# Kernel optimization log

Hardware: AMD Instinct MI355X
Metric: run time of the kernel (lower is better)

## Reference

```python
import jax, jax.numpy as jnp
import numpy as np

SIZE = 1024      # codebook entries
CODE_DIM = 256   # embedding dim


def setup_inputs() -> dict:
    key = jax.random.key(0)
    k_z, k_w = jax.random.split(key)
    z = jax.random.normal(k_z, (8, CODE_DIM, 16, 32, 32), dtype=jnp.float32)
    # init.uniform_(weight, -1/size, 1/size)
    codebook = jax.random.uniform(
        k_w, (SIZE, CODE_DIM), dtype=jnp.float32,
        minval=-1.0 / SIZE, maxval=1.0 / SIZE)
    return {"z": z, "codebook": codebook}


def reference(z, codebook):
    bs, d, t, h, w = z.shape
    # tokens: [N, d] with N = bs*t*h*w (matches permute(0,2,3,4,1).reshape(-1,d))
    zf = jnp.transpose(z, (0, 2, 3, 4, 1)).reshape(-1, d)
    # squared-distance expansion instead of materializing [size, N, d]:
    # ||z - e||^2 = ||z||^2 - 2 z.e + ||e||^2 ; argmin identical to argmin of norm
    d2 = (jnp.sum(zf * zf, axis=1, keepdims=True)
          - 2.0 * (zf @ codebook.T)
          + jnp.sum(codebook * codebook, axis=1))  # [N, size]
    encoding_indices = jnp.argmin(d2, axis=-1).reshape(bs, t, h, w)
    # gather + permute back to [bs, d, t, h, w]
    quantized = jnp.transpose(codebook[encoding_indices], (0, 4, 1, 2, 3))
    st = z + jax.lax.stop_gradient(quantized - z)  # straight-through output
    return (quantized, st, encoding_indices)
```

## Files before the change

### kernel.cpp

```cpp
#include <hip/hip_runtime.h>
#include <stdint.h>


constexpr int Dd  = 256;
constexpr int SPB = 16384;
constexpr int Nn  = 131072;
constexpr int Kk  = 1024;
constexpr int CCAP = 16;
#define WWIN 2.2e-3f

typedef short short8 __attribute__((ext_vector_type(8)));
typedef float v4f    __attribute__((ext_vector_type(4)));

__device__ __forceinline__ unsigned bf16pk(float a, float b){
  unsigned ua = __float_as_uint(a), ub = __float_as_uint(b);
  ua = (ua + 0x7fffu + ((ua >> 16) & 1u)) >> 16;
  ub = (ub + 0x7fffu + ((ub >> 16) & 1u)) & 0xffff0000u;
  return ua | ub;
}
__device__ __forceinline__ short8 frg(uint4 u){
  union { uint4 a; short8 b; } x; x.a = u; return x.b;
}
__device__ __forceinline__ v4f mfma16(short8 a, short8 b, v4f c){
  return __builtin_amdgcn_mfma_f32_16x16x32_bf16(a, b, c, 0, 0, 0);
}
__device__ __forceinline__ void dma16(const void* g, void* l){
  __builtin_amdgcn_global_load_lds((const __attribute__((address_space(1))) void*)g,
                                   (__attribute__((address_space(3))) void*)l, 16, 0, 0);
}

__global__ __launch_bounds__(64) void cnorm_k(const float* __restrict__ cb,
                                              float* __restrict__ cn){
  const int k = blockIdx.x, l = threadIdx.x;
  const float* row = cb + (size_t)k * Dd;
  float s = 0.f;
  #pragma unroll
  for (int c = 0; c < Dd; c += 64){ float v = row[c + l]; s += v * v; }
  #pragma unroll
  for (int off = 32; off > 0; off >>= 1) s += __shfl_down(s, off, 64);
  if (l == 0) cn[k] = s;
}

__global__ __launch_bounds__(256) void cconv_k(const float* __restrict__ cb,
                                               uint4* __restrict__ Bg){
  const int cc = blockIdx.x, n = threadIdx.x;
  const float* row = cb + (size_t)(cc * 256 + n) * Dd;
  for (int dc = 0; dc < 8; dc++){
    float v[32];
    const float4* rp = (const float4*)(row + dc * 32);
    #pragma unroll
    for (int q = 0; q < 8; q++){
      float4 f = rp[q]; v[4*q]=f.x; v[4*q+1]=f.y; v[4*q+2]=f.z; v[4*q+3]=f.w;
    }
    unsigned hv[16];
    #pragma unroll
    for (int p = 0; p < 16; p++) hv[p] = bf16pk(v[2*p], v[2*p+1]);
    size_t base = ((size_t)cc * 8 + dc) * 1024;
    #pragma unroll
    for (int kq = 0; kq < 4; kq++)
      Bg[base + (size_t)kq*256 + n] = make_uint4(hv[4*kq],hv[4*kq+1],hv[4*kq+2],hv[4*kq+3]);
  }
}

__device__ __forceinline__ void epi(const v4f (&acc)[4], const int c,
                                    const int li, const int lq, const int w,
                                    const int tok0, const float* cnS,
                                    unsigned (&bestR)[4], unsigned (&thrU)[4],
                                    int (&cntR)[4],
                                    unsigned short* __restrict__ candW){
  float cnv[4];
  #pragma unroll
  for (int ni = 0; ni < 4; ni++) cnv[ni] = cnS[c*64 + ni*16 + li];
  const int codeB = c*64 + li;
  #pragma unroll
  for (int r = 0; r < 4; r++){
    unsigned pv[4];
    unsigned pm = 0xFFFFFFFFu;
    #pragma unroll
    for (int ni = 0; ni < 4; ni++){
      float s = fmaf(acc[ni][r], -2.0f, cnv[ni]);
      unsigned u = __float_as_uint(s);
      u ^= (unsigned)((int)u >> 31) | 0x80000000u;
      unsigned p = (u & 0xFFFFFC00u) | (unsigned)(codeB + ni*16);
      pv[ni] = p;
      pm = (pm < p) ? pm : p;
    }
    unsigned pmw = pm;
    #pragma unroll
    for (int off = 1; off < 16; off <<= 1){
      unsigned o = (unsigned)__shfl_xor((int)pmw, off, 16);
      pmw = (pmw < o) ? pmw : o;
    }
    if (pmw <= bestR[r]){
      bestR[r] = pmw;
      unsigned bp = pmw & 0xFFFFFC00u;
      unsigned fb = (bp & 0x80000000u) ? (bp ^ 0x80000000u) : ~bp;
      float thrf = __uint_as_float(fb) + WWIN;
      unsigned tu = __float_as_uint(thrf);
      tu ^= (unsigned)((int)tu >> 31) | 0x80000000u;
      thrU[r] = tu | 1023u;
    }
    if (__any(pm <= thrU[r])){
      const int tok = tok0 + w*16 + lq*4 + r;
      int base = cntR[r];
      #pragma unroll
      for (int ni = 0; ni < 4; ni++){
        const unsigned p = pv[ni];
        const bool pass = (p <= thrU[r]);
        unsigned long long bal = __ballot(pass);
        const unsigned bq = (unsigned)(bal >> (lq*16)) & 0xFFFFu;
        if (pass){
          int pos = base + __popc(bq & ((1u << li) - 1u));
          if (pos < CCAP)
            candW[(size_t)tok*CCAP + pos] = (unsigned short)(p & 1023u);
        }
        base += __popc(bq);
      }
      cntR[r] = base;
    }
  }
}

__global__ __launch_bounds__(512, 4) void vq_sweep_k(const float* __restrict__ z,
                                                     const uint4* __restrict__ Bg,
                                                     const float* __restrict__ cnG,
                                                     int* __restrict__ cntW,
                                                     unsigned short* __restrict__ candW,
                                                     int* __restrict__ abestW,
                                                     int* __restrict__ hCntB,
                                                     int* __restrict__ heavyRegion,
                                                     int* __restrict__ idsW,
                                                     float* __restrict__ out){
  __shared__ uint4 Bs[2][2048];
  __shared__ float cnS[1024];
  __shared__ int hN;
  __shared__ int hT[128];

  const int tid = threadIdx.x, bId = blockIdx.x;
  const int w = tid >> 6, ln = tid & 63;
  const int li = ln & 15, lq = ln >> 4;

  if (tid == 0) hN = 0;

  if (w < 4) dma16((const uint4*)cnG + w*64 + ln, (uint4*)&cnS[w*256]);
  int bOff[4];
  #pragma unroll
  for (int j = 0; j < 4; j++){
    const int f = j*512 + tid;
    bOff[j] = (f >> 8)*1024 + ((f >> 6) & 3)*256 + (f & 63);
  }
  #pragma unroll
  for (int j = 0; j < 4; j++)
    dma16(Bg + bOff[j], &Bs[0][j*512 + w*64]);

  const int tok0 = bId * 128;
  const int b = tok0 >> 14;
  const int s0 = tok0 & 16383;
  const float* zb = z + (size_t)b * Dd * SPB + s0;
  short8 aF[8];
  const int tl = w*16 + li;
  #pragma unroll
  for (int kk = 0; kk < 8; kk++){
    float v[8];
    #pragma unroll
    for (int j = 0; j < 8; j++)
      v[j] = zb[(size_t)(kk*32 + lq*8 + j) * SPB + tl];
    union { unsigned u[4]; short8 s8; } x;
    #pragma unroll
    for (int p = 0; p < 4; p++) x.u[p] = bf16pk(v[2*p], v[2*p+1]);
    aF[kk] = x.s8;
  }

  unsigned bestR[4], thrU[4]; int cntR[4];
  #pragma unroll
  for (int i = 0; i < 4; i++){ bestR[i] = 0xFFFFFFFFu; thrU[i] = 0u; cntR[i] = 0; }

  v4f accA[4], accB[4];
  const v4f vz = {0.f, 0.f, 0.f, 0.f};

  for (int cp = 0; cp < 8; cp++){
    const int c0 = cp*2, c1 = c0 + 1;

    {
      const int cn1 = c0 + 1;
      const int srcB = (cn1 >> 2)*8192 + (cn1 & 3)*64;
      #pragma unroll
      for (int j = 0; j < 4; j++)
        dma16(Bg + srcB + bOff[j], &Bs[1][j*512 + w*64]);
      asm volatile("s_waitcnt vmcnt(4)" ::: "memory");
      __builtin_amdgcn_s_barrier();
      asm volatile("" ::: "memory");

      #pragma unroll
      for (int ni = 0; ni < 4; ni++) accA[ni] = vz;
      const uint4* Bbase = &Bs[0][lq*64 + li];
      __builtin_amdgcn_s_setprio(1);
      #pragma unroll
      for (int kk = 0; kk < 8; kk++){
        short8 b0 = frg(Bbase[kk*256 +  0]);
        short8 b1 = frg(Bbase[kk*256 + 16]);
        short8 b2 = frg(Bbase[kk*256 + 32]);
        short8 b3 = frg(Bbase[kk*256 + 48]);
        accA[0] = mfma16(aF[kk], b0, accA[0]);
        accA[1] = mfma16(aF[kk], b1, accA[1]);
        accA[2] = mfma16(aF[kk], b2, accA[2]);
        accA[3] = mfma16(aF[kk], b3, accA[3]);
      }
      __builtin_amdgcn_s_setprio(0);
      if (cp)
        epi(accB, c0 - 1, li, lq, w, tok0, cnS, bestR, thrU, cntR, candW);
      __builtin_amdgcn_s_barrier();
      asm volatile("" ::: "memory");
    }

    {
      if (c1 < 15){
        const int cn1 = c1 + 1;
        const int srcB = (cn1 >> 2)*8192 + (cn1 & 3)*64;
        #pragma unroll
        for (int j = 0; j < 4; j++)
          dma16(Bg + srcB + bOff[j], &Bs[0][j*512 + w*64]);
        asm volatile("s_waitcnt vmcnt(4)" ::: "memory");
      } else {
        asm volatile("s_waitcnt vmcnt(0)" ::: "memory");
      }
      __builtin_amdgcn_s_barrier();
      asm volatile("" ::: "memory");

      #pragma unroll
      for (int ni = 0; ni < 4; ni++) accB[ni] = vz;
      const uint4* Bbase = &Bs[1][lq*64 + li];
      __builtin_amdgcn_s_setprio(1);
      #pragma unroll
      for (int kk = 0; kk < 8; kk++){
        short8 b0 = frg(Bbase[kk*256 +  0]);
        short8 b1 = frg(Bbase[kk*256 + 16]);
        short8 b2 = frg(Bbase[kk*256 + 32]);
        short8 b3 = frg(Bbase[kk*256 + 48]);
        accB[0] = mfma16(aF[kk], b0, accB[0]);
        accB[1] = mfma16(aF[kk], b1, accB[1]);
        accB[2] = mfma16(aF[kk], b2, accB[2]);
        accB[3] = mfma16(aF[kk], b3, accB[3]);
      }
      __builtin_amdgcn_s_setprio(0);
      epi(accA, c0, li, lq, w, tok0, cnS, bestR, thrU, cntR, candW);
      __builtin_amdgcn_s_barrier();
      asm volatile("" ::: "memory");
    }
  }
  epi(accB, 15, li, lq, w, tok0, cnS, bestR, thrU, cntR, candW);

  if (li == 0){
    #pragma unroll
    for (int r = 0; r < 4; r++){
      const int tok = tok0 + w*16 + lq*4 + r;
      if (cntR[r] == 1){
        const int code = (int)(bestR[r] & 1023u);
        idsW[tok] = code;
        out[(size_t)2 * Nn * Dd + tok] = (float)code;
      } else {
        int p = atomicAdd(&hN, 1);
        hT[p] = tok;
        cntW[tok] = cntR[r];
        abestW[tok] = (int)(bestR[r] & 1023u);
      }
    }
  }
  __syncthreads();
  if (tid == 0) hCntB[bId] = hN;
  if (tid < hN) heavyRegion[bId*128 + tid] = hT[tid];
}

__global__ __launch_bounds__(256) void vq_finish_k(const float* __restrict__ z,
                                                   const float* __restrict__ cb,
                                                   const float* __restrict__ cnG,
                                                   const int* __restrict__ cntW,
                                                   const unsigned short* __restrict__ candW,
                                                   const int* __restrict__ abestW,
                                                   const int* __restrict__ hCntB,
                                                   const int* __restrict__ heavyRegion,
                                                   const int* __restrict__ idsW,
                                                   float* __restrict__ out){
  __shared__ __align__(16) float smem[64*129];
  __shared__ int idS[128];

  const int tid = threadIdx.x, reg = blockIdx.x;
  const int tok0 = reg * 128;
  const int b = tok0 >> 14, sb = tok0 & 16383;

  if (tid < 128) idS[tid] = idsW[tok0 + tid];

  const int h = hCntB[reg];
  if (h > 0){
    float* zS = smem;
    const float* zb = z + (size_t)b * Dd * SPB + sb;

    const bool act = tid < h;
    int tok = 0, tl = 0, n = 0, abest = 0;
    bool ovf = false;
    unsigned short cds[CCAP];
    if (act){
      tok = heavyRegion[reg*128 + tid];
      tl = tok & 127;
      n = cntW[tok];
      ovf = (n > CCAP);
      if (ovf) n = CCAP;
      *(uint4*)&cds[0] = *(const uint4*)&candW[(size_t)tok * CCAP];
      *(uint4*)&cds[8] = *(const uint4*)&candW[(size_t)tok * CCAP + 8];
      abest = abestW[tok];
    }
    const int eIdx = act ? (ovf ? abest : (int)cds[0]) : 0;

    float accs[CCAP];
    #pragma unroll
    for (int i = 0; i < CCAP; i++) accs[i] = 0.f;
    float accE = 0.f, za = 0.f;

    for (int ch = 0; ch < 4; ch++){
      if (ch) __syncthreads();
      #pragma unroll
      for (int rr = 0; rr < 8; rr++){
        const int f4 = rr*256 + tid;
        const int row = f4 >> 5, c4 = f4 & 31;
        const float4 v = *(const float4*)(zb + (size_t)(ch*64 + row) * SPB + c4*4);
        *(float4*)&zS[row*128 + c4*4] = v;
      }
      __syncthreads();
      if (act){
        #pragma unroll 8
        for (int d = 0; d < 64; d++){
          const float v = zS[d*128 + tl];
          za = fmaf(v, v, za);
        }
        #pragma unroll
        for (int ci = 0; ci < CCAP; ci++){
          if (ci < n){
            const float* cr = cb + (size_t)cds[ci] * Dd + ch*64;
            float a = accs[ci];
            #pragma unroll
            for (int d = 0; d < 64; d += 4){
              const float4 cv = *(const float4*)(cr + d);
              a = fmaf(zS[(d+0)*128 + tl], cv.x, a);
              a = fmaf(zS[(d+1)*128 + tl], cv.y, a);
              a = fmaf(zS[(d+2)*128 + tl], cv.z, a);
              a = fmaf(zS[(d+3)*128 + tl], cv.w, a);
            }
            accs[ci] = a;
          }
        }
        if (ovf){
          const float* cr = cb + (size_t)eIdx * Dd + ch*64;
          float a = accE;
          #pragma unroll
          for (int d = 0; d < 64; d += 4){
            const float4 cv = *(const float4*)(cr + d);
            a = fmaf(zS[(d+0)*128 + tl], cv.x, a);
            a = fmaf(zS[(d+1)*128 + tl], cv.y, a);
            a = fmaf(zS[(d+2)*128 + tl], cv.z, a);
            a = fmaf(zS[(d+3)*128 + tl], cv.w, a);
          }
          accE = a;
        }
      }
    }

    if (act){
      float bv = 3.4e38f; int bi = 0x7fffffff;
      #pragma unroll
      for (int ci = 0; ci < CCAP; ci++){
        if (ci < n){
          const int ix = (int)cds[ci];
          float t  = za - 2.0f * accs[ci];
          float d2 = t + cnG[ix];
          if (d2 < bv || (d2 == bv && ix < bi)){ bv = d2; bi = ix; }
        }
      }
      if (ovf){
        float t  = za - 2.0f * accE;
        float d2 = t + cnG[eIdx];
        if (d2 < bv || (d2 == bv && eIdx < bi)){ bv = d2; bi = eIdx; }
      }
      idS[tl] = bi;
      out[(size_t)2 * Nn * Dd + tok] = (float)bi;
    }
  }
  __syncthreads();

  float* tile = smem;
  const int r2 = tid >> 7, ccol = tid & 127;
  const int s = tid & 63, cq = tid >> 6;
  for (int hh = 0; hh < 2; hh++){
    const int s0h = hh * 64;
    float* qb  = out + (size_t)b * Dd * SPB + sb + s0h + s;
    float* stb = qb + (size_t)Nn * Dd;
    for (int ch = 0; ch < 2; ch++){
      if (hh | ch) __syncthreads();
      #pragma unroll 4
      for (int t0 = 0; t0 < 64; t0 += 2){
        const int row = t0 + r2;
        tile[row*129 + ccol] = cb[(size_t)idS[s0h + row] * Dd + ch*128 + ccol];
      }
      __syncthreads();
      #pragma unroll 8
      for (int i = 0; i < 32; i++){
        const int cc2 = i*4 + cq;
        const float v = tile[s*129 + cc2];
        const size_t off = (size_t)(ch*128 + cc2) * SPB;
        qb[off]  = v;
        stb[off] = v;
      }
    }
  }
}

#define MICRO_STEP(WITH_ZN)                                                    \
    {                                                                          \
        float4 a0 = *(const float4*)&As[d][ty * 8];                            \
        float4 a1 = *(const float4*)&As[d][ty * 8 + 4];                        \
        float4 b0 = *(const float4*)&Bs[d][tx * 8];                            \
        float4 b1 = *(const float4*)&Bs[d][tx * 8 + 4];                        \
        float a[8] = {a0.x, a0.y, a0.z, a0.w, a1.x, a1.y, a1.z, a1.w};         \
        float bb[8] = {b0.x, b0.y, b0.z, b0.w, b1.x, b1.y, b1.z, b1.w};        \
        _Pragma("unroll")                                                      \
        for (int i = 0; i < 8; i++) {                                          \
            _Pragma("unroll")                                                  \
            for (int j = 0; j < 8; j++) acc[i][j] += a[i] * bb[j];             \
            if (WITH_ZN) zn[i] += a[i] * a[i];                                 \
        }                                                                      \
    }

__global__ __launch_bounds__(256) void vq_k(const float* __restrict__ z,
                                            const float* __restrict__ cb,
                                            const float* __restrict__ cn,
                                            float* __restrict__ out){
  __shared__ float As[16][128];
  __shared__ float Bs[16][132];
  __shared__ int   idsf[128];
  const int tid = threadIdx.x;
  const int tx = tid & 15, ty = tid >> 4;
  const int blk = blockIdx.x;
  const int b = blk >> 7, sb = (blk & 127) * 128;
  const float* zb = z + (size_t)b * Dd * SPB + sb;
  float bestv[8]; int besti[8]; float zn[8];
  #pragma unroll
  for (int i = 0; i < 8; i++){ bestv[i] = 3.4e38f; besti[i] = 0; zn[i] = 0.f; }
  const int am = tid & 127, ad = tid >> 7;
  const int bd = tid & 15,  bk = tid >> 4;
  for (int cc = 0; cc < 8; cc++){
    float acc[8][8];
    #pragma unroll
    for (int i = 0; i < 8; i++)
      #pragma unroll
      for (int j = 0; j < 8; j++) acc[i][j] = 0.f;
    for (int dc = 0; dc < 16; dc++){
      #pragma unroll
      for (int r = 0; r < 8; r++){
        const int d = ad + r * 2;
        As[d][am] = zb[(size_t)(dc*16 + d) * SPB + am];
      }
      #pragma unroll
      for (int r = 0; r < 8; r++){
        const int k = bk + r * 16;
        Bs[bd][k] = cb[(size_t)(cc*128 + k) * Dd + dc*16 + bd];
      }
      __syncthreads();
      if (cc == 0){
        #pragma unroll
        for (int d = 0; d < 16; d++) MICRO_STEP(1)
      } else {
        #pragma unroll
        for (int d = 0; d < 16; d++) MICRO_STEP(0)
      }
      __syncthreads();
    }
    const float* cnp = cn + cc*128 + tx*8;
    float4 c0 = *(const float4*)cnp;
    float4 c1 = *(const float4*)(cnp + 4);
    float cv[8] = {c0.x, c0.y, c0.z, c0.w, c1.x, c1.y, c1.z, c1.w};
    #pragma unroll
    for (int i = 0; i < 8; i++){
      #pragma unroll
      for (int j = 0; j < 8; j++){
        float t  = zn[i] - 2.0f * acc[i][j];
        float d2 = t + cv[j];
        int   ix = cc*128 + tx*8 + j;
        if (d2 < bestv[i]){ bestv[i] = d2; besti[i] = ix; }
      }
    }
  }
  #pragma unroll
  for (int i = 0; i < 8; i++){
    float v = bestv[i]; int ix = besti[i];
    #pragma unroll
    for (int off = 8; off > 0; off >>= 1){
      float ov = __shfl_down(v, off, 16);
      int   oi = __shfl_down(ix, off, 16);
      if (ov < v || (ov == v && oi < ix)){ v = ov; ix = oi; }
    }
    if (tx == 0) idsf[ty*8 + i] = ix;
  }
  __syncthreads();
  if (tid < 128) out[(size_t)2*Nn*Dd + (size_t)blk*128 + tid] = (float)idsf[tid];
  const int m = tid & 127, cg = tid >> 7;
  const int myidx = idsf[m];
  const float* crow = cb + (size_t)myidx * Dd + cg*128;
  float* q  = out + (size_t)b * Dd * SPB + (size_t)cg * 128 * SPB + sb + m;
  float* st = q + (size_t)Nn * Dd;
  #pragma unroll 8
  for (int r = 0; r < 128; r++){
    const float v = crow[r];
    q[(size_t)r * SPB]  = v;
    st[(size_t)r * SPB] = v;
  }
}

extern "C" void kernel_launch(void* const* d_in, const int* in_sizes, int n_in,
                              void* d_out, int out_size, void* d_ws, size_t ws_size,
                              hipStream_t stream){
  const float* z  = (const float*)d_in[0];
  const float* cb = (const float*)d_in[1];
  float* out = (float*)d_out;

  const size_t BG_B  = (size_t)4 * 8 * 1024 * 16;
  const size_t CN_B  = (size_t)Kk * 4;
  const size_t CNT_B = (size_t)Nn * 4;
  const size_t CAN_B = (size_t)Nn * CCAP * 2;
  const size_t ABW_B = (size_t)Nn * 4;
  const size_t IDS_B = (size_t)Nn * 4;
  const size_t HCB_B = (size_t)(Nn/128) * 4;
  const size_t HR_B  = (size_t)Nn * 4;
  const size_t NEED = BG_B + CN_B + CNT_B + CAN_B + ABW_B + IDS_B + HCB_B + HR_B;

  if (ws_size >= NEED){
    uint8_t* ws = (uint8_t*)d_ws;
    size_t o = 0;
    uint4* Bg   = (uint4*)(ws + o);          o += BG_B;
    float* cnG  = (float*)(ws + o);          o += CN_B;
    int*   cntW = (int*)(ws + o);            o += CNT_B;
    unsigned short* candW = (unsigned short*)(ws + o); o += CAN_B;
    int*   abW  = (int*)(ws + o);            o += ABW_B;
    int*   idsW = (int*)(ws + o);            o += IDS_B;
    int*   hCB  = (int*)(ws + o);            o += HCB_B;
    int*   hReg = (int*)(ws + o);            o += HR_B;

    cnorm_k<<<Kk, 64, 0, stream>>>(cb, cnG);
    cconv_k<<<4, 256, 0, stream>>>(cb, Bg);
    vq_sweep_k<<<Nn/128, 512, 0, stream>>>(z, Bg, cnG, cntW, candW, abW,
                                           hCB, hReg, idsW, out);
    vq_finish_k<<<Nn/128, 256, 0, stream>>>(z, cb, cnG, cntW, candW, abW,
                                            hCB, hReg, idsW, out);
  } else {
    float* cn = (float*)d_ws;
    cnorm_k<<<Kk, 64, 0, stream>>>(cb, cn);
    vq_k<<<Nn/128, 256, 0, stream>>>(z, cb, cn, out);
  }
}
```

Measured before the change: 597.8 us.

## Drop heavy-token compaction lists and vectorize quantized output stores

The sweep kernel no longer compacts ambiguous tokens into per-block heavy lists with a shared atomic counter and an extra barrier. It now writes every token's candidate count, and the finish kernel detects per-block whether any token needs refinement by reading those counts directly. The output write loop is also reorganized so each thread gathers four consecutive spatial positions from the shared tile and emits float4 stores instead of scalar stores. This removes the atomic, a barrier and the list writes, at the cost of writing counts for all tokens and having refinement use token-indexed threads.

```diff
diff --git a/kernel.cpp b/kernel.cpp
--- a/kernel.cpp
+++ b/kernel.cpp
@@ -127,20 +127,14 @@
                                                      int* __restrict__ cntW,
                                                      unsigned short* __restrict__ candW,
                                                      int* __restrict__ abestW,
-                                                     int* __restrict__ hCntB,
-                                                     int* __restrict__ heavyRegion,
                                                      int* __restrict__ idsW,
                                                      float* __restrict__ out){
   __shared__ uint4 Bs[2][2048];
   __shared__ float cnS[1024];
-  __shared__ int hN;
-  __shared__ int hT[128];
 
   const int tid = threadIdx.x, bId = blockIdx.x;
   const int w = tid >> 6, ln = tid & 63;
   const int li = ln & 15, lq = ln >> 4;
-
-  if (tid == 0) hN = 0;
 
   if (w < 4) dma16((const uint4*)cnG + w*64 + ln, (uint4*)&cnS[w*256]);
   int bOff[4];
@@ -254,21 +248,16 @@
     #pragma unroll
     for (int r = 0; r < 4; r++){
       const int tok = tok0 + w*16 + lq*4 + r;
+      cntW[tok] = cntR[r];
       if (cntR[r] == 1){
         const int code = (int)(bestR[r] & 1023u);
         idsW[tok] = code;
         out[(size_t)2 * Nn * Dd + tok] = (float)code;
       } else {
-        int p = atomicAdd(&hN, 1);
-        hT[p] = tok;
-        cntW[tok] = cntR[r];
         abestW[tok] = (int)(bestR[r] & 1023u);
       }
     }
   }
-  __syncthreads();
-  if (tid == 0) hCntB[bId] = hN;
-  if (tid < hN) heavyRegion[bId*128 + tid] = hT[tid];
 }
 
 __global__ __launch_bounds__(256) void vq_finish_k(const float* __restrict__ z,
@@ -277,32 +266,38 @@
                                                    const int* __restrict__ cntW,
                                                    const unsigned short* __restrict__ candW,
                                                    const int* __restrict__ abestW,
-                                                   const int* __restrict__ hCntB,
-                                                   const int* __restrict__ heavyRegion,
                                                    const int* __restrict__ idsW,
                                                    float* __restrict__ out){
   __shared__ __align__(16) float smem[64*129];
   __shared__ int idS[128];
+  __shared__ int anyH;
 
   const int tid = threadIdx.x, reg = blockIdx.x;
   const int tok0 = reg * 128;
   const int b = tok0 >> 14, sb = tok0 & 16383;
 
-  if (tid < 128) idS[tid] = idsW[tok0 + tid];
-
-  const int h = hCntB[reg];
-  if (h > 0){
+  if (tid == 0) anyH = 0;
+  int cntL = 0;
+  if (tid < 128){
+    idS[tid] = idsW[tok0 + tid];
+    cntL = cntW[tok0 + tid];
+  }
+  __syncthreads();
+  const bool act = (cntL > 1);
+  if (act) anyH = 1;
+  __syncthreads();
+
+  if (anyH){
     float* zS = smem;
     const float* zb = z + (size_t)b * Dd * SPB + sb;
 
-    const bool act = tid < h;
-    int tok = 0, tl = 0, n = 0, abest = 0;
+    const int tok = tok0 + tid;
+    const int tl = tid;
+    int n = 0, abest = 0;
     bool ovf = false;
     unsigned short cds[CCAP];
     if (act){
-      tok = heavyRegion[reg*128 + tid];
-      tl = tok & 127;
-      n = cntW[tok];
+      n = cntL;
       ovf = (n > CCAP);
       if (ovf) n = CCAP;
       *(uint4*)&cds[0] = *(const uint4*)&candW[(size_t)tok * CCAP];
@@ -388,10 +383,10 @@
 
   float* tile = smem;
   const int r2 = tid >> 7, ccol = tid & 127;
-  const int s = tid & 63, cq = tid >> 6;
+  const int s4 = tid & 15, d16 = tid >> 4;
   for (int hh = 0; hh < 2; hh++){
     const int s0h = hh * 64;
-    float* qb  = out + (size_t)b * Dd * SPB + sb + s0h + s;
+    float* qb  = out + (size_t)b * Dd * SPB + sb + s0h + s4*4;
     float* stb = qb + (size_t)Nn * Dd;
     for (int ch = 0; ch < 2; ch++){
       if (hh | ch) __syncthreads();
@@ -401,13 +396,17 @@
         tile[row*129 + ccol] = cb[(size_t)idS[s0h + row] * Dd + ch*128 + ccol];
       }
       __syncthreads();
-      #pragma unroll 8
-      for (int i = 0; i < 32; i++){
-        const int cc2 = i*4 + cq;
-        const float v = tile[s*129 + cc2];
-        const size_t off = (size_t)(ch*128 + cc2) * SPB;
-        qb[off]  = v;
-        stb[off] = v;
+      #pragma unroll
+      for (int k = 0; k < 8; k++){
+        const int dcol = d16 + 16*k;
+        float4 v;
+        v.x = tile[(s4*4 + 0)*129 + dcol];
+        v.y = tile[(s4*4 + 1)*129 + dcol];
+        v.z = tile[(s4*4 + 2)*129 + dcol];
+        v.w = tile[(s4*4 + 3)*129 + dcol];
+        const size_t off = (size_t)(ch*128 + dcol) * SPB;
+        *(float4*)(qb  + off) = v;
+        *(float4*)(stb + off) = v;
       }
     }
   }
@@ -527,9 +526,7 @@
   const size_t CAN_B = (size_t)Nn * CCAP * 2;
   const size_t ABW_B = (size_t)Nn * 4;
   const size_t IDS_B = (size_t)Nn * 4;
-  const size_t HCB_B = (size_t)(Nn/128) * 4;
-  const size_t HR_B  = (size_t)Nn * 4;
-  const size_t NEED = BG_B + CN_B + CNT_B + CAN_B + ABW_B + IDS_B + HCB_B + HR_B;
+  const size_t NEED = BG_B + CN_B + CNT_B + CAN_B + ABW_B + IDS_B;
 
   if (ws_size >= NEED){
     uint8_t* ws = (uint8_t*)d_ws;
@@ -540,15 +537,13 @@
     unsigned short* candW = (unsigned short*)(ws + o); o += CAN_B;
     int*   abW  = (int*)(ws + o);            o += ABW_B;
     int*   idsW = (int*)(ws + o);            o += IDS_B;
-    int*   hCB  = (int*)(ws + o);            o += HCB_B;
-    int*   hReg = (int*)(ws + o);            o += HR_B;
 
     cnorm_k<<<Kk, 64, 0, stream>>>(cb, cnG);
     cconv_k<<<4, 256, 0, stream>>>(cb, Bg);
     vq_sweep_k<<<Nn/128, 512, 0, stream>>>(z, Bg, cnG, cntW, candW, abW,
-                                           hCB, hReg, idsW, out);
+                                           idsW, out);
     vq_finish_k<<<Nn/128, 256, 0, stream>>>(z, cb, cnG, cntW, candW, abW,
-                                            hCB, hReg, idsW, out);
+                                            idsW, out);
   } else {
     float* cn = (float*)d_ws;
     cnorm_k<<<Kk, 64, 0, stream>>>(cb, cn);
```

Result: no change. 593.6 us (-0.7%).
